# Performance work log

Hardware: AMD Instinct MI355X
Metric: run time of the kernel (lower is better)

Reference implementation:

```python
import jax, jax.numpy as jnp
import numpy as np

L = 7  # window size (odd)
A = 0.1
B_COEF = 0.9


def mex_hat(d):
    grid = (np.mgrid[:d, :d] - d // 2) * 1.0
    eucl = (grid ** 2).sum(0) ** 0.5
    eucl /= d
    return eucl * np.exp(-eucl)


def setup_inputs() -> dict:
    key = jax.random.key(0)
    x = jax.random.normal(key, (16, 1, 512, 512), dtype=jnp.float32)
    kernel = jnp.asarray(mex_hat(L).reshape(-1), dtype=jnp.float32)  # [49], row-major like unfold
    return {"x": x, "kernel": kernel}


def reference(x, kernel):
    # x: [B,1,H,W], kernel: [L*L]
    # Extract zero-padded LxL patches, matching F.unfold(padding=L//2) ordering
    # (C=1, kernel positions row-major). patches: [B, L*L, H, W]
    patches = jax.lax.conv_general_dilated_patches(
        x, (L, L), (1, 1), 'SAME')
    average_term = jnp.exp(-patches.mean(axis=1, keepdims=True))  # [B,1,H,W]
    differential_term = jnp.sum(
        kernel[None, :, None, None] * jax.nn.relu(patches - x),
        axis=1, keepdims=True)  # [B,1,H,W]
    suppression = A * average_term + B_COEF * differential_term
    norm = jnp.sqrt(jnp.sum(suppression ** 2))
    suppression = suppression / norm
    mask = jnp.where(x > suppression, jnp.ones_like(x), jnp.zeros_like(x))
    return mask, average_term, differential_term
```

## Files before the change

kernel.cpp:

```cpp
#include <hip/hip_runtime.h>
#include <math.h>

#define HW 512
#define NB 16
#define TX 64
#define TY 64
#define LDSW 72
#define LDSH 70
#define N_PIX (NB * HW * HW)
#define NBLK (8 * 8 * NB)

__device__ __forceinline__ float sgpr_f(float v) {
    return __uint_as_float(__builtin_amdgcn_readfirstlane(__float_as_uint(v)));
}

__global__ __launch_bounds__(256, 4) void li_phase1(
    const float* __restrict__ x, const float* __restrict__ kw,
    float* __restrict__ out_ratio, float* __restrict__ out_avg,
    float* __restrict__ out_dif, float* __restrict__ partials)
{
    __shared__ float tile[LDSH * LDSW];
    __shared__ float wsum[4];

    const int tid = threadIdx.x;
    const int bx = blockIdx.x, by = blockIdx.y, b = blockIdx.z;
    const int x0 = bx * TX, y0 = by * TY;
    const float* xb = x + (size_t)b * (HW * HW);

    float w[49];
    float W = 0.f;
#pragma unroll
    for (int i = 0; i < 49; i++) { w[i] = sgpr_f(kw[i]); W += w[i]; }

    for (int idx = tid; idx < LDSH * (LDSW / 4); idx += 256) {
        int r = idx / (LDSW / 4);
        int c4 = idx - r * (LDSW / 4);
        int gy = y0 - 3 + r;
        int gx = x0 - 4 + c4 * 4;
        float4 v = make_float4(0.f, 0.f, 0.f, 0.f);
        if ((unsigned)gy < HW && (unsigned)gx < HW)
            v = *(const float4*)(xb + gy * HW + gx);
        *(float4*)&tile[r * LDSW + c4 * 4] = v;
    }
    __syncthreads();

    const int tx  = tid & 63;
    const int ty0 = (tid >> 6) * 16;

    float cen[16];
#pragma unroll
    for (int p = 0; p < 16; p++)
        cen[p] = tile[(ty0 + p + 3) * LDSW + tx + 4];

    float dif[16], bsum[16];
#pragma unroll
    for (int p = 0; p < 16; p++) { dif[p] = 0.f; bsum[p] = 0.f; }

    const size_t base = (size_t)b * (HW * HW) + (size_t)(y0 + ty0) * HW + x0 + tx;
    float ss = 0.f;

    float vc[7], vn[7];
#pragma unroll
    for (int dj = 0; dj < 7; dj++)
        vc[dj] = tile[ty0 * LDSW + tx + 1 + dj];

#pragma unroll
    for (int r = 0; r < 22; r++) {
        if (r < 21) {
#pragma unroll
            for (int dj = 0; dj < 7; dj++)
                vn[dj] = tile[(ty0 + r + 1) * LDSW + tx + 1 + dj];
        }

        float rs = ((vc[0] + vc[1]) + (vc[2] + vc[3])) + ((vc[4] + vc[5]) + vc[6]);
#pragma unroll
        for (int p = 0; p < 16; p++) {
            const int di = r - p;
            if (di >= 0 && di < 7) {
                bsum[p] += rs;
#pragma unroll
                for (int dj = 0; dj < 7; dj++) {
                    if (di == 3 && dj == 3) continue;
                    dif[p] = fmaf(w[di * 7 + dj], fmaxf(vc[dj], cen[p]), dif[p]);
                }
            }
        }

        if (r >= 6) {
            const int p = r - 6;
            float avg = __expf(-bsum[p] * (1.0f / 49.0f));
            float d = fmaf(-W, cen[p], dif[p]);
            float sp = 0.1f * avg + 0.9f * d;
            size_t gi = base + (size_t)p * HW;
            __builtin_nontemporal_store(avg, out_avg + gi);
            __builtin_nontemporal_store(d,   out_dif + gi);
            out_ratio[gi] = cen[p] * __builtin_amdgcn_rcpf(sp);
            ss = fmaf(sp, sp, ss);
        }

#pragma unroll
        for (int dj = 0; dj < 7; dj++) vc[dj] = vn[dj];
    }

#pragma unroll
    for (int off = 32; off > 0; off >>= 1)
        ss += __shfl_down(ss, off, 64);
    if ((tid & 63) == 0) wsum[tid >> 6] = ss;
    __syncthreads();
    if (tid == 0)
        partials[bx + 8 * (by + 8 * b)] = (wsum[0] + wsum[1]) + (wsum[2] + wsum[3]);
}

__global__ __launch_bounds__(256) void li_phase2(
    const float* __restrict__ partials, float* __restrict__ io)
{
    __shared__ float wsum[4];
    __shared__ float s_inv;
    const int tid = threadIdx.x;

    float s = 0.f;
#pragma unroll
    for (int i = 0; i < NBLK / 256; i++)
        s += partials[tid + i * 256];
#pragma unroll
    for (int off = 32; off > 0; off >>= 1)
        s += __shfl_down(s, off, 64);
    if ((tid & 63) == 0) wsum[tid >> 6] = s;
    __syncthreads();
    if (tid == 0)
        s_inv = 1.0f / sqrtf((wsum[0] + wsum[1]) + (wsum[2] + wsum[3]));
    __syncthreads();

    const float inv = s_inv;
    const int base = blockIdx.x * 4096 + tid * 4;
#pragma unroll
    for (int k = 0; k < 4; k++) {
        const int i = base + k * 1024;
        float4 r = *(const float4*)(io + i);
        float4 m;
        m.x = (r.x > inv) ? 1.f : 0.f;
        m.y = (r.y > inv) ? 1.f : 0.f;
        m.z = (r.z > inv) ? 1.f : 0.f;
        m.w = (r.w > inv) ? 1.f : 0.f;
        *(float4*)(io + i) = m;
    }
}

extern "C" void kernel_launch(void* const* d_in, const int* in_sizes, int n_in,
                              void* d_out, int out_size, void* d_ws, size_t ws_size,
                              hipStream_t stream) {
    const float* x  = (const float*)d_in[0];
    const float* kw = (const float*)d_in[1];
    float* out   = (float*)d_out;
    float* ratio = out;
    float* avg   = out + N_PIX;
    float* dif   = out + 2 * (size_t)N_PIX;
    float* ws    = (float*)d_ws;

    dim3 g(HW / TX, HW / TY, NB);
    li_phase1<<<g, 256, 0, stream>>>(x, kw, ratio, avg, dif, ws);
    li_phase2<<<N_PIX / 4096, 256, 0, stream>>>(ws, ratio);
}
```

Baseline: 97.32 us.

## Fuse normalization pass into main kernel with grid-wide atomic barrier

Merges the two kernels into one persistent-style kernel. Each block publishes its partial sum of squares, increments a global counter and spins until all 512 blocks arrive, then computes the norm and writes the mask straight from the ratios held in registers. This removes the second launch and the read-back and rewrite of the ratio array. To make all blocks co-resident it doubles the tile height (32 rows per thread) and lowers the occupancy hint to 2. It also adds a memset for the counter, and it risks deadlock if not all blocks can be resident, plus heavy register pressure.

```diff
diff --git a/kernel.cpp b/kernel.cpp
--- a/kernel.cpp
+++ b/kernel.cpp
@@ -4,23 +4,25 @@
 #define HW 512
 #define NB 16
 #define TX 64
-#define TY 64
+#define TY 128
 #define LDSW 72
-#define LDSH 70
+#define LDSH 134
 #define N_PIX (NB * HW * HW)
-#define NBLK (8 * 8 * NB)
+#define NBLK (8 * 4 * NB)
 
 __device__ __forceinline__ float sgpr_f(float v) {
     return __uint_as_float(__builtin_amdgcn_readfirstlane(__float_as_uint(v)));
 }
 
-__global__ __launch_bounds__(256, 4) void li_phase1(
+__global__ __launch_bounds__(256, 2) void li_fused(
     const float* __restrict__ x, const float* __restrict__ kw,
-    float* __restrict__ out_ratio, float* __restrict__ out_avg,
-    float* __restrict__ out_dif, float* __restrict__ partials)
+    float* __restrict__ out_mask, float* __restrict__ out_avg,
+    float* __restrict__ out_dif, float* __restrict__ partials,
+    unsigned int* __restrict__ ctr)
 {
     __shared__ float tile[LDSH * LDSW];
     __shared__ float wsum[4];
+    __shared__ float s_inv;
 
     const int tid = threadIdx.x;
     const int bx = blockIdx.x, by = blockIdx.y, b = blockIdx.z;
@@ -45,16 +47,14 @@
     __syncthreads();
 
     const int tx  = tid & 63;
-    const int ty0 = (tid >> 6) * 16;
+    const int ty0 = (tid >> 6) * 32;
 
-    float cen[16];
+    float cen[32], dif[32], bsum[32], ratio[32];
 #pragma unroll
-    for (int p = 0; p < 16; p++)
+    for (int p = 0; p < 32; p++) {
         cen[p] = tile[(ty0 + p + 3) * LDSW + tx + 4];
-
-    float dif[16], bsum[16];
-#pragma unroll
-    for (int p = 0; p < 16; p++) { dif[p] = 0.f; bsum[p] = 0.f; }
+        dif[p] = 0.f; bsum[p] = 0.f;
+    }
 
     const size_t base = (size_t)b * (HW * HW) + (size_t)(y0 + ty0) * HW + x0 + tx;
     float ss = 0.f;
@@ -65,8 +65,8 @@
         vc[dj] = tile[ty0 * LDSW + tx + 1 + dj];
 
 #pragma unroll
-    for (int r = 0; r < 22; r++) {
-        if (r < 21) {
+    for (int r = 0; r < 38; r++) {
+        if (r < 37) {
 #pragma unroll
             for (int dj = 0; dj < 7; dj++)
                 vn[dj] = tile[(ty0 + r + 1) * LDSW + tx + 1 + dj];
@@ -74,7 +74,7 @@
 
         float rs = ((vc[0] + vc[1]) + (vc[2] + vc[3])) + ((vc[4] + vc[5]) + vc[6]);
 #pragma unroll
-        for (int p = 0; p < 16; p++) {
+        for (int p = 0; p < 32; p++) {
             const int di = r - p;
             if (di >= 0 && di < 7) {
                 bsum[p] += rs;
@@ -92,9 +92,9 @@
             float d = fmaf(-W, cen[p], dif[p]);
             float sp = 0.1f * avg + 0.9f * d;
             size_t gi = base + (size_t)p * HW;
-            __builtin_nontemporal_store(avg, out_avg + gi);
-            __builtin_nontemporal_store(d,   out_dif + gi);
-            out_ratio[gi] = cen[p] * __builtin_amdgcn_rcpf(sp);
+            out_avg[gi] = avg;
+            out_dif[gi] = d;
+            ratio[p] = cen[p] * __builtin_amdgcn_rcpf(sp);
             ss = fmaf(sp, sp, ss);
         }
 
@@ -107,21 +107,23 @@
         ss += __shfl_down(ss, off, 64);
     if ((tid & 63) == 0) wsum[tid >> 6] = ss;
     __syncthreads();
-    if (tid == 0)
-        partials[bx + 8 * (by + 8 * b)] = (wsum[0] + wsum[1]) + (wsum[2] + wsum[3]);
-}
+    if (tid == 0) {
+        const int flat = bx + 8 * (by + 4 * b);
+        __hip_atomic_store(&partials[flat],
+                           (wsum[0] + wsum[1]) + (wsum[2] + wsum[3]),
+                           __ATOMIC_RELAXED, __HIP_MEMORY_SCOPE_AGENT);
+        __hip_atomic_fetch_add(ctr, 1u, __ATOMIC_RELEASE,
+                               __HIP_MEMORY_SCOPE_AGENT);
+        while (__hip_atomic_load(ctr, __ATOMIC_ACQUIRE,
+                                 __HIP_MEMORY_SCOPE_AGENT) < NBLK)
+            __builtin_amdgcn_s_sleep(8);
+    }
+    __syncthreads();
 
-__global__ __launch_bounds__(256) void li_phase2(
-    const float* __restrict__ partials, float* __restrict__ io)
-{
-    __shared__ float wsum[4];
-    __shared__ float s_inv;
-    const int tid = threadIdx.x;
-
-    float s = 0.f;
-#pragma unroll
-    for (int i = 0; i < NBLK / 256; i++)
-        s += partials[tid + i * 256];
+    float s = __hip_atomic_load(&partials[tid], __ATOMIC_RELAXED,
+                                __HIP_MEMORY_SCOPE_AGENT)
+            + __hip_atomic_load(&partials[tid + 256], __ATOMIC_RELAXED,
+                                __HIP_MEMORY_SCOPE_AGENT);
 #pragma unroll
     for (int off = 32; off > 0; off >>= 1)
         s += __shfl_down(s, off, 64);
@@ -132,18 +134,9 @@
     __syncthreads();
 
     const float inv = s_inv;
-    const int base = blockIdx.x * 4096 + tid * 4;
 #pragma unroll
-    for (int k = 0; k < 4; k++) {
-        const int i = base + k * 1024;
-        float4 r = *(const float4*)(io + i);
-        float4 m;
-        m.x = (r.x > inv) ? 1.f : 0.f;
-        m.y = (r.y > inv) ? 1.f : 0.f;
-        m.z = (r.z > inv) ? 1.f : 0.f;
-        m.w = (r.w > inv) ? 1.f : 0.f;
-        *(float4*)(io + i) = m;
-    }
+    for (int p = 0; p < 32; p++)
+        out_mask[base + (size_t)p * HW] = (ratio[p] > inv) ? 1.f : 0.f;
 }
 
 extern "C" void kernel_launch(void* const* d_in, const int* in_sizes, int n_in,
@@ -151,13 +144,15 @@
                               hipStream_t stream) {
     const float* x  = (const float*)d_in[0];
     const float* kw = (const float*)d_in[1];
-    float* out   = (float*)d_out;
-    float* ratio = out;
-    float* avg   = out + N_PIX;
-    float* dif   = out + 2 * (size_t)N_PIX;
-    float* ws    = (float*)d_ws;
+    float* out  = (float*)d_out;
+    float* mask = out;
+    float* avg  = out + N_PIX;
+    float* dif  = out + 2 * (size_t)N_PIX;
+    float* partials = (float*)d_ws;
+    unsigned int* ctr = (unsigned int*)d_ws + NBLK;
+
+    hipMemsetAsync(ctr, 0, sizeof(unsigned int), stream);
 
     dim3 g(HW / TX, HW / TY, NB);
-    li_phase1<<<g, 256, 0, stream>>>(x, kw, ratio, avg, dif, ws);
-    li_phase2<<<N_PIX / 4096, 256, 0, stream>>>(ws, ratio);
+    li_fused<<<g, 256, 0, stream>>>(x, kw, mask, avg, dif, partials, ctr);
 }
```

Result: slower. 331.2 us (+240.3%).
